# Kernel optimization log

Measured on AMD Instinct MI355X. Metric: run time of the kernel, lower is better.

## Reference

```python
import jax, jax.numpy as jnp
import numpy as np

BN_EPS = 1e-5
EPS = 1e-6


def _conv(x, w, pad, dil):
    # NCHW dilated conv, stride 1, no bias (matches nn.Conv2d(bias=False))
    return jax.lax.conv_general_dilated(
        x, w, window_strides=(1, 1), padding=[(pad, pad), (pad, pad)],
        rhs_dilation=(dil, dil), dimension_numbers=('NCHW', 'OIHW', 'NCHW'))


def _bn_relu(x, s, b, m, v):
    # eval-mode batchnorm (running stats) + relu
    inv = (s / jnp.sqrt(v + BN_EPS))[None, :, None, None]
    return jax.nn.relu((x - m[None, :, None, None]) * inv + b[None, :, None, None])


def _l2n(x):
    # l2_norm over channel dim (dim=-2 of [B,C,N]); no eps, as in source
    return x / jnp.linalg.norm(x, axis=1, keepdims=True)


def _forward(x, w1, w2, w3, w4, bn_scale, bn_bias, bn_mean, bn_var,
             wq, bq, wk, bk, wv, bv, gamma):
    B, C, H, W = x.shape
    N = H * W
    # HASP: four dilated-conv branches (dilations 1,6,12,18), concat to 128 ch
    specs = [(w1, 0, 1), (w2, 6, 6), (w3, 12, 12), (w4, 18, 18)]
    branches = [_bn_relu(_conv(x, w, p, d), bn_scale[i], bn_bias[i],
                         bn_mean[i], bn_var[i])
                for i, (w, p, d) in enumerate(specs)]
    x_q = jnp.concatenate(branches, axis=1)  # [B,128,H,W]
    # 1x1 convs as channel GEMMs
    Q = (jnp.einsum('oi,bihw->bohw', wq[:, :, 0, 0], x_q)
         + bq[None, :, None, None]).reshape(B, -1, N)  # [B,16,N]
    K = (jnp.einsum('oi,bihw->bohw', wk[:, :, 0, 0], x)
         + bk[None, :, None, None]).reshape(B, -1, N)  # [B,16,N]
    V = (jnp.einsum('oi,bihw->bohw', wv[:, :, 0, 0], x)
         + bv[None, :, None, None]).reshape(B, -1, N)  # [B,128,N]
    Qn = _l2n(Q).transpose(0, 2, 1)  # [B,N,16]
    Kn = _l2n(K)                     # [B,16,N]
    tailor = 1.0 / (N + jnp.einsum('bnm,bm->bn', Qn, Kn.sum(-1) + EPS))  # [B,N]
    vsum = V.sum(-1)[:, :, None]                      # [B,128,1]
    mat = jnp.einsum('bmn,bcn->bmc', Kn, V)           # [B,16,128]
    msum = vsum + jnp.einsum('bnm,bmc->bcn', Qn, mat)  # [B,128,N]
    out = (msum * tailor[:, None, :]).reshape(B, C, H, W)
    return gamma * out


def setup_inputs() -> dict:
    key = jax.random.key(0)
    ks = jax.random.split(key, 12)
    B, C, H, W = 8, 128, 128, 128
    M = 16  # in_places // scale
    d = {
        'x': jax.random.normal(ks[0], (B, C, H, W), jnp.float32),
        'w1': jax.random.normal(ks[1], (32, 128, 1, 1), jnp.float32) * 0.05,
        'w2': jax.random.normal(ks[2], (32, 128, 3, 3), jnp.float32) * 0.05,
        'w3': jax.random.normal(ks[3], (32, 128, 3, 3), jnp.float32) * 0.05,
        'w4': jax.random.normal(ks[4], (32, 128, 3, 3), jnp.float32) * 0.05,
        'bn_scale': jnp.ones((4, 32), jnp.float32),
        'bn_bias': jnp.zeros((4, 32), jnp.float32),
        'bn_mean': jnp.zeros((4, 32), jnp.float32),
        'bn_var': jnp.ones((4, 32), jnp.float32),
        'wq': jax.random.normal(ks[5], (M, 128, 1, 1), jnp.float32) * 0.05,
        'bq': jax.random.normal(ks[6], (M,), jnp.float32) * 0.05,
        'wk': jax.random.normal(ks[7], (M, 128, 1, 1), jnp.float32) * 0.05,
        'bk': jax.random.normal(ks[8], (M,), jnp.float32) * 0.05,
        'wv': jax.random.normal(ks[9], (C, 128, 1, 1), jnp.float32) * 0.05,
        'bv': jax.random.normal(ks[10], (C,), jnp.float32) * 0.05,
        'gamma': jax.random.uniform(ks[11], (1,), jnp.float32),
    }
    return d


def reference(x, w1, w2, w3, w4, bn_scale, bn_bias, bn_mean, bn_var,
              wq, bq, wk, bk, wv, bv, gamma):
    return _forward(x, w1, w2, w3, w4, bn_scale, bn_bias, bn_mean, bn_var,
                    wq, bq, wk, bk, wv, bv, gamma)
```

## Files before the change

kernel.cpp:

```cpp
#include <hip/hip_runtime.h>
#include <hip/hip_bf16.h>
#include <math.h>

#define NPIX   16384
#define BATCH  8
#define BN_EPS 1e-5f
#define EPS_V  1e-6f

typedef __attribute__((ext_vector_type(8))) short bf16x8;
typedef __attribute__((ext_vector_type(4))) float f32x4;
typedef const __attribute__((address_space(1))) unsigned int* gas_ptr;
typedef __attribute__((address_space(3))) unsigned int* las_ptr;

#define OFF_K     ((size_t)0)
#define OFF_PART2 ((size_t)8192)
#define OFF_W1F   ((size_t)2097152)
#define OFF_WKT   ((size_t)2101248)
#define OFF_WVT   ((size_t)2103296)
#define OFF_BF    ((size_t)2119680)
#define OFF_PART  ((size_t)2119808)
#define OFF_STATS ((size_t)3242112)
#define BASE_END  ((size_t)3259648)
#define OFF_WBT   BASE_END
#define OFF_XT    ((size_t)3314976)
#define OFF_WVB   ((size_t)11703584)
#define OFF_ZROW  ((size_t)11711776)
#define NEW_END   ((size_t)11713824)
#define OFF_W24T  BASE_END

__device__ inline unsigned short f2bf(float f) {
  union { float f; unsigned int u; } v; v.f = f;
  unsigned int r = (v.u + 0x7FFFu + ((v.u >> 16) & 1u)) >> 16;
  return (unsigned short)r;
}

__global__ void prep_common_kernel(const float* __restrict__ w1,
                                   const float* __restrict__ bns, const float* __restrict__ bnb,
                                   const float* __restrict__ bnm, const float* __restrict__ bnv,
                                   const float* __restrict__ wk, const float* __restrict__ wv,
                                   float* __restrict__ w1f, float* __restrict__ wkt,
                                   float* __restrict__ wvt, float* __restrict__ bf) {
  int tid = blockIdx.x * blockDim.x + threadIdx.x;
  int nt  = gridDim.x * blockDim.x;
  for (int i = tid; i < 128; i += nt) {
    float inv = bns[i] * rsqrtf(bnv[i] + BN_EPS);
    bf[i] = bnb[i] - bnm[i] * inv;
  }
  for (int i = tid; i < 4096; i += nt) {
    int c = i >> 5, o = i & 31;
    float inv = bns[o] * rsqrtf(bnv[o] + BN_EPS);
    w1f[i] = w1[o * 128 + c] * inv;
  }
  for (int i = tid; i < 2048; i += nt) {
    int c = i >> 4, m = i & 15;
    wkt[i] = wk[m * 128 + c];
  }
  for (int i = tid; i < 16384; i += nt) {
    int c = i >> 7, o = i & 127;
    wvt[i] = wv[o * 128 + c];
  }
}

__global__ void prep_convb_kernel(const float* __restrict__ w1,
                                  const float* __restrict__ w2, const float* __restrict__ w3,
                                  const float* __restrict__ w4,
                                  const float* __restrict__ bns, const float* __restrict__ bnv,
                                  const float* __restrict__ wk, const float* __restrict__ wv,
                                  unsigned short* __restrict__ wbtr,
                                  unsigned short* __restrict__ wvbr,
                                  unsigned short* __restrict__ wxbr,
                                  unsigned short* __restrict__ zrow) {
  int tid = blockIdx.x * blockDim.x + threadIdx.x;
  int nt  = gridDim.x * blockDim.x;
  for (int i = tid; i < 4096; i += nt) zrow[i] = 0;
  for (int i = tid; i < 16384; i += nt) {
    int e = i & 7, lane = (i >> 3) & 63, f = (i >> 9) & 7, q = i >> 12;
    int oc = f * 16 + (lane & 15);
    int c  = q * 32 + (lane >> 4) * 8 + e;
    wvbr[i] = f2bf(wv[oc * 128 + c]);
  }
  for (int i = tid; i < 6144; i += nt) {
    int e = i & 7, lane = (i >> 3) & 63, ct = i >> 9;
    int tile = ct % 3, q = ct / 3;
    int c = q * 32 + (lane >> 4) * 8 + e;
    float val;
    if (tile < 2) {
      int oc = tile * 16 + (lane & 15);
      val = w1[oc * 128 + c] * (bns[oc] * rsqrtf(bnv[oc] + BN_EPS));
    } else {
      val = wk[(lane & 15) * 128 + c];
    }
    wxbr[i] = f2bf(val);
  }
  for (int i = tid; i < 110592; i += nt) {
    int br = i / 36864;
    int r  = i - br * 36864;
    int tap  = r >> 12;
    int r2   = r & 4095;
    int q    = r2 >> 10;
    int r3   = r2 & 1023;
    int pair = r3 >> 9;
    int r4   = r3 & 511;
    int lane = r4 >> 3, e = r4 & 7;
    int oc = pair * 16 + (lane & 15);
    int c  = q * 32 + (lane >> 4) * 8 + e;
    const float* w = (br == 0) ? w2 : ((br == 1) ? w3 : w4);
    int bo = (br + 1) * 32 + oc;
    float inv = bns[bo] * rsqrtf(bnv[bo] + BN_EPS);
    wbtr[i] = f2bf(w[(oc * 128 + c) * 9 + tap] * inv);
  }
}

__global__ void prep_convf_kernel(const float* __restrict__ w2, const float* __restrict__ w3,
                                  const float* __restrict__ w4,
                                  const float* __restrict__ bns, const float* __restrict__ bnv,
                                  float* __restrict__ w24t) {
  int tid = blockIdx.x * blockDim.x + threadIdx.x;
  int nt  = gridDim.x * blockDim.x;
  for (int i = tid; i < 110592; i += nt) {
    int br  = i / 36864;
    int rem = i - br * 36864;
    int c   = rem / 288;
    int k   = (rem % 288) >> 5;
    int o   = rem & 31;
    const float* w = (br == 0) ? w2 : ((br == 1) ? w3 : w4);
    int bo = (br + 1) * 32 + o;
    float inv = bns[bo] * rsqrtf(bnv[bo] + BN_EPS);
    w24t[i] = w[(o * 128 + c) * 9 + k] * inv;
  }
}

__global__ __launch_bounds__(256) void a0_kernel(const float* __restrict__ x,
                                                 unsigned short* __restrict__ xt) {
  __shared__ unsigned short Ts[64][132];
  int t   = threadIdx.x;
  int b   = blockIdx.y;
  int px0 = blockIdx.x * 64;
  const float* xb = x + (size_t)b * 128 * NPIX;
  int p = t & 63, cq = t >> 6;
#pragma unroll 8
  for (int i = 0; i < 32; ++i) {
    int c = cq * 32 + i;
    Ts[p][c] = f2bf(xb[(size_t)c * NPIX + px0 + p]);
  }
  __syncthreads();
  int pw = t >> 2, cg = t & 3;
  unsigned short* dst = xt + ((size_t)(b * 4 + cg) * 16384 + px0 + pw) * 32;
  int sw = (pw >> 1) & 3;
#pragma unroll
  for (int k = 0; k < 8; ++k) {
    uint2 v = *(const uint2*)(&Ts[pw][cg * 32 + k * 4]);
    int cgs = (k >> 1) ^ sw;
    *(uint2*)(dst + cgs * 8 + (k & 1) * 4) = v;
  }
}

__global__ __launch_bounds__(256) void a1_kernel(const float* __restrict__ x,
                                                 const float* __restrict__ w1f,
                                                 const float* __restrict__ wkt,
                                                 const float* __restrict__ bfp,
                                                 const float* __restrict__ bk,
                                                 float* __restrict__ out,
                                                 float* __restrict__ Kbuf) {
  __shared__ float lw1[128 * 32];
  __shared__ float lwk[128 * 16];
  __shared__ float lbf[32];
  int t = threadIdx.x;
  for (int i = t; i < 4096; i += 256) lw1[i] = w1f[i];
  for (int i = t; i < 2048; i += 256) lwk[i] = wkt[i];
  if (t < 32) lbf[t] = bfp[t];
  __syncthreads();

  int b  = blockIdx.y;
  int px = blockIdx.x * 256 + t;
  const float* xb = x + (size_t)b * 128 * NPIX;

  float acc[48];
#pragma unroll
  for (int i = 0; i < 48; ++i) acc[i] = 0.f;

  for (int c = 0; c < 128; ++c) {
    float xv = xb[(size_t)c * NPIX + px];
    const float4* w1p = (const float4*)(lw1 + c * 32);
#pragma unroll
    for (int j = 0; j < 8; ++j) {
      float4 w = w1p[j];
      acc[j*4+0] = fmaf(w.x, xv, acc[j*4+0]);
      acc[j*4+1] = fmaf(w.y, xv, acc[j*4+1]);
      acc[j*4+2] = fmaf(w.z, xv, acc[j*4+2]);
      acc[j*4+3] = fmaf(w.w, xv, acc[j*4+3]);
    }
    const float4* wkp = (const float4*)(lwk + c * 16);
#pragma unroll
    for (int j = 0; j < 4; ++j) {
      float4 w = wkp[j];
      acc[32+j*4+0] = fmaf(w.x, xv, acc[32+j*4+0]);
      acc[32+j*4+1] = fmaf(w.y, xv, acc[32+j*4+1]);
      acc[32+j*4+2] = fmaf(w.z, xv, acc[32+j*4+2]);
      acc[32+j*4+3] = fmaf(w.w, xv, acc[32+j*4+3]);
    }
  }
#pragma unroll
  for (int o = 0; o < 32; ++o)
    out[((size_t)(b * 128 + o)) * NPIX + px] = fmaxf(acc[o] + lbf[o], 0.f);
#pragma unroll
  for (int m = 0; m < 16; ++m)
    Kbuf[((size_t)(b * 16 + m)) * NPIX + px] = acc[32 + m] + bk[m];
}

__global__ __launch_bounds__(256) void a2m_kernel(const unsigned short* __restrict__ xt,
                                                  const unsigned short* __restrict__ zrow,
                                                  const unsigned short* __restrict__ wbtr,
                                                  const float* __restrict__ bfp,
                                                  float* __restrict__ out) {
  __shared__ unsigned short sx[3 * 8192 + 8];
  int t    = threadIdx.x;
  int wave = t >> 6, lane = t & 63;
  int l15  = lane & 15, cg = lane >> 4;
  int idx  = blockIdx.x;
  int b    = idx & 7;
  int rest = idx >> 3;
  int h2   = rest & 63;
  int br   = rest >> 6;
  int d    = 6 * (br + 1);
  int h0   = h2 * 2;
  int j    = wave >> 1;
  int whalf = wave & 1;
  int p0   = whalf * 64;

  if (t == 0) *(uint4*)(sx + 24576) = make_uint4(0u, 0u, 0u, 0u);

  const unsigned short* wb    = wbtr + (size_t)br * 36864;
  const unsigned short* slabs = xt + (size_t)b * 4 * 524288;

  f32x4 acc[2][4];
#pragma unroll
  for (int i = 0; i < 2; ++i)
#pragma unroll
    for (int n = 0; n < 4; ++n) acc[i][n] = (f32x4){0.f, 0.f, 0.f, 0.f};

  int pxb[3], xorv[3];
#pragma unroll
  for (int kw = 0; kw < 3; ++kw) {
    pxb[kw]  = p0 + l15 + (kw - 1) * d;
    xorv[kw] = (cg ^ ((pxb[kw] >> 1) & 3)) << 4;
  }

  auto STAGE = [&](int s) {
    int q = s / 3, kh = s % 3;
    int srow = h0 + j + (kh - 1) * d;
    const unsigned short* rowsrc =
        ((unsigned)srow < 128u) ? (slabs + (size_t)q * 524288 + (size_t)srow * 4096)
                                : zrow;
    const unsigned short* gsrc = rowsrc + whalf * 2048 + lane * 8;
    unsigned short* lbase = sx + (s % 3) * 8192 + j * 4096 + whalf * 2048;
#pragma unroll
    for (int k = 0; k < 4; ++k)
      __builtin_amdgcn_global_load_lds((gas_ptr)(const void*)(gsrc + k * 512),
                                       (las_ptr)(void*)(lbase + k * 512), 16, 0, 0);
  };

  auto COMPUTE = [&](int s) {
    int q = s / 3, kh = s % 3;
    int bb = (s % 3) * 16384 + j * 8192;
    bf16x8 a[3][2];
#pragma unroll
    for (int kw = 0; kw < 3; ++kw) {
      int tap = kh * 3 + kw;
      const unsigned short* wt = wb + ((((size_t)tap * 4 + q) * 2) << 9);
      a[kw][0] = *(const bf16x8*)(wt + lane * 8);
      a[kw][1] = *(const bf16x8*)(wt + 512 + lane * 8);
    }
#pragma unroll
    for (int kw = 0; kw < 3; ++kw) {
      int base = bb + pxb[kw] * 64 + xorv[kw];
#pragma unroll
      for (int nf = 0; nf < 4; ++nf) {
        int px   = pxb[kw] + nf * 16;
        int addr = ((unsigned)px < 128u) ? (base + nf * 1024) : 49152;
        bf16x8 bv = *(const bf16x8*)((const char*)sx + addr);
        acc[0][nf] = __builtin_amdgcn_mfma_f32_16x16x32_bf16(a[kw][0], bv, acc[0][nf], 0, 0, 0);
        acc[1][nf] = __builtin_amdgcn_mfma_f32_16x16x32_bf16(a[kw][1], bv, acc[1][nf], 0, 0, 0);
      }
    }
  };

  STAGE(0);
  STAGE(1);
  __syncthreads();
  for (int s = 0; s < 12; ++s) {
    COMPUTE(s);
    if (s < 10) STAGE(s + 2);
    if (s < 11) {
      if (s < 10) asm volatile("s_waitcnt vmcnt(4)" ::: "memory");
      else        asm volatile("s_waitcnt vmcnt(0)" ::: "memory");
      __builtin_amdgcn_s_barrier();
      __builtin_amdgcn_sched_barrier(0);
    }
  }

  int ocb = (br + 1) * 32;
  int pxw = (h0 + j) * 128 + p0;
#pragma unroll
  for (int mf = 0; mf < 2; ++mf) {
#pragma unroll
    for (int r = 0; r < 4; ++r) {
      int oc = mf * 16 + cg * 4 + r;
      float bias = bfp[ocb + oc];
      float* op = out + ((size_t)(b * 128 + ocb + oc)) * NPIX + pxw + l15;
#pragma unroll
      for (int nf = 0; nf < 4; ++nf)
        op[nf * 16] = fmaxf(acc[mf][nf][r] + bias, 0.f);
    }
  }
}

__global__ __launch_bounds__(256) void a2f_kernel(const float* __restrict__ x,
                                                  const float* __restrict__ w24t,
                                                  const float* __restrict__ bfp,
                                                  float* __restrict__ out) {
  int t  = threadIdx.x;
  int og = t & 3;
  int pg = (t >> 2) & 15;
  int r  = t >> 6;
  int br = blockIdx.z;
  int b  = blockIdx.y;
  int h  = blockIdx.x * 4 + r;
  int d  = 6 * (br + 1);

  const float* wt = w24t + (size_t)br * 36864;
  const float* bf = bfp + (br + 1) * 32;
  const float* xb = x + (size_t)b * 128 * NPIX;
  int w0 = pg << 3;

  float acc[8][8];
#pragma unroll
  for (int p = 0; p < 8; ++p)
#pragma unroll
    for (int o = 0; o < 8; ++o) acc[p][o] = 0.f;

  for (int c = 0; c < 128; ++c) {
    const float* xc = xb + (size_t)c * NPIX;
    const float* wc = wt + c * 288;
#pragma unroll
    for (int kh = 0; kh < 3; ++kh) {
      int row = h + (kh - 1) * d;
      if ((unsigned)row >= 128u) continue;
      const float* xr = xc + row * 128;
#pragma unroll
      for (int kw = 0; kw < 3; ++kw) {
        int wb = w0 + (kw - 1) * d;
        float xv[8];
        if (wb >= 0 && wb <= 120) {
          const float2* p2 = (const float2*)(xr + wb);
#pragma unroll
          for (int jj = 0; jj < 4; ++jj) {
            float2 v = p2[jj];
            xv[2*jj] = v.x; xv[2*jj+1] = v.y;
          }
        } else {
#pragma unroll
          for (int jj = 0; jj < 8; ++jj) {
            int ww = wb + jj;
            xv[jj] = ((unsigned)ww < 128u) ? xr[ww] : 0.f;
          }
        }
        const float4* wp = (const float4*)(wc + (kh * 3 + kw) * 32 + og * 8);
        float4 wa = wp[0], wbv = wp[1];
        float wr[8] = {wa.x, wa.y, wa.z, wa.w, wbv.x, wbv.y, wbv.z, wbv.w};
#pragma unroll
        for (int p = 0; p < 8; ++p)
#pragma unroll
          for (int o = 0; o < 8; ++o)
            acc[p][o] = fmaf(xv[p], wr[o], acc[p][o]);
      }
    }
  }

  int chbase = (br + 1) * 32 + og * 8;
  int n = h * 128 + w0;
#pragma unroll
  for (int o = 0; o < 8; ++o) {
    float bias = bf[og * 8 + o];
    float* op = out + ((size_t)(b * 128 + chbase + o)) * NPIX + n;
    float4 v0 = make_float4(fmaxf(acc[0][o] + bias, 0.f), fmaxf(acc[1][o] + bias, 0.f),
                            fmaxf(acc[2][o] + bias, 0.f), fmaxf(acc[3][o] + bias, 0.f));
    float4 v1 = make_float4(fmaxf(acc[4][o] + bias, 0.f), fmaxf(acc[5][o] + bias, 0.f),
                            fmaxf(acc[6][o] + bias, 0.f), fmaxf(acc[7][o] + bias, 0.f));
    ((float4*)op)[0] = v0;
    ((float4*)op)[1] = v1;
  }
}

__global__ __launch_bounds__(256) void cm_kernel(const unsigned short* __restrict__ xt,
                                                 const unsigned short* __restrict__ wvbr,
                                                 const unsigned short* __restrict__ wxbr,
                                                 const float* __restrict__ bv,
                                                 const float* __restrict__ bfp,
                                                 const float* __restrict__ bk,
                                                 float* __restrict__ out,
                                                 float* __restrict__ part1,
                                                 float* __restrict__ part2) {
  __shared__ __align__(16) unsigned short Vl[128 * 136];
  __shared__ __align__(16) unsigned short knl[16 * 136];
  int t    = threadIdx.x;
  int idx  = blockIdx.x;
  int b    = idx & 7;
  int blk  = idx >> 3;
  int wave = t >> 6, lane = t & 63;
  int l15  = lane & 15, cg = lane >> 4;
  int ocb  = wave * 32;
  int pbase = blk << 7;
  int cgsw = (cg ^ ((l15 >> 1) & 3)) << 3;

  float bvr[2][4];
#pragma unroll
  for (int mf = 0; mf < 2; ++mf)
#pragma unroll
    for (int r = 0; r < 4; ++r) bvr[mf][r] = bv[ocb + mf * 16 + cg * 4 + r];

  float xb4[4];
#pragma unroll
  for (int r = 0; r < 4; ++r) xb4[r] = 0.f;
  if (wave == 0) {
#pragma unroll
    for (int r = 0; r < 4; ++r) xb4[r] = bfp[cg * 4 + r];
  } else if (wave == 1) {
#pragma unroll
    for (int r = 0; r < 4; ++r) xb4[r] = bfp[16 + cg * 4 + r];
  } else if (wave == 2) {
#pragma unroll
    for (int r = 0; r < 4; ++r) xb4[r] = bk[cg * 4 + r];
  }
  int xwave = (wave < 3) ? wave : 0;

  float kr[4] = {0.f, 0.f, 0.f, 0.f};
  float sv[2][4];
#pragma unroll
  for (int mf = 0; mf < 2; ++mf)
#pragma unroll
    for (int r = 0; r < 4; ++r) sv[mf][r] = 0.f;
  f32x4 am[2];
  am[0] = (f32x4){0.f,0.f,0.f,0.f};
  am[1] = (f32x4){0.f,0.f,0.f,0.f};

#pragma unroll
  for (int hf = 0; hf < 2; ++hf) {
    f32x4 vacc[2][4];
    f32x4 xacc[4];
#pragma unroll
    for (int i = 0; i < 2; ++i)
#pragma unroll
      for (int n = 0; n < 4; ++n) vacc[i][n] = (f32x4){0.f,0.f,0.f,0.f};
#pragma unroll
    for (int n = 0; n < 4; ++n) xacc[n] = (f32x4){0.f,0.f,0.f,0.f};

#pragma unroll
    for (int cc = 0; cc < 4; ++cc) {
      const unsigned short* xq = xt + ((size_t)(b * 4 + cc) * 16384 + pbase) * 32;
      bf16x8 a0 = *(const bf16x8*)(wvbr + ((cc * 8 + wave * 2 + 0) << 9) + lane * 8);
      bf16x8 a1 = *(const bf16x8*)(wvbr + ((cc * 8 + wave * 2 + 1) << 9) + lane * 8);
      bf16x8 ax = *(const bf16x8*)(wxbr + ((cc * 3 + xwave) << 9) + lane * 8);
#pragma unroll
      for (int nf = 0; nf < 4; ++nf) {
        int nfg = hf * 4 + nf;
        bf16x8 bx = *(const bf16x8*)(xq + (size_t)(nfg * 16 + l15) * 32 + cgsw);
        vacc[0][nf] = __builtin_amdgcn_mfma_f32_16x16x32_bf16(a0, bx, vacc[0][nf], 0, 0, 0);
        vacc[1][nf] = __builtin_amdgcn_mfma_f32_16x16x32_bf16(a1, bx, vacc[1][nf], 0, 0, 0);
        if (wave < 3)
          xacc[nf] = __builtin_amdgcn_mfma_f32_16x16x32_bf16(ax, bx, xacc[nf], 0, 0, 0);
      }
    }

#pragma unroll
    for (int mf = 0; mf < 2; ++mf) {
#pragma unroll
      for (int r = 0; r < 4; ++r) {
        float s = 0.f;
#pragma unroll
        for (int nf = 0; nf < 4; ++nf) s += vacc[mf][nf][r];
        sv[mf][r] += s;
        int c = ocb + mf * 16 + cg * 4 + r;
#pragma unroll
        for (int nf = 0; nf < 4; ++nf)
          Vl[c * 136 + (hf * 4 + nf) * 16 + l15] = f2bf(vacc[mf][nf][r] + bvr[mf][r]);
      }
    }

    if (wave < 2) {
#pragma unroll
      for (int r = 0; r < 4; ++r) {
        int oc = wave * 16 + cg * 4 + r;
        float* op = out + ((size_t)(b * 128 + oc)) * NPIX + pbase + l15;
#pragma unroll
        for (int nf = 0; nf < 4; ++nf)
          op[(hf * 4 + nf) * 16] = fmaxf(xacc[nf][r] + xb4[r], 0.f);
      }
    } else if (wave == 2) {
#pragma unroll
      for (int nf = 0; nf < 4; ++nf) {
        int nfg = hf * 4 + nf;
        float kq[4]; float s2 = 0.f;
#pragma unroll
        for (int r = 0; r < 4; ++r) {
          kq[r] = xacc[nf][r] + xb4[r];
          s2 = fmaf(kq[r], kq[r], s2);
        }
        s2 += __shfl_xor(s2, 16);
        s2 += __shfl_xor(s2, 32);
        float inv = rsqrtf(s2);
#pragma unroll
        for (int r = 0; r < 4; ++r) {
          float kn = kq[r] * inv;
          knl[(cg * 4 + r) * 136 + nfg * 16 + l15] = f2bf(kn);
          kr[r] += kn;
        }
      }
    }
  }
  __syncthreads();

#pragma unroll
  for (int ks = 0; ks < 4; ++ks) {
    bf16x8 af = *(const bf16x8*)(knl + l15 * 136 + ks * 32 + cg * 8);
    bf16x8 b0 = *(const bf16x8*)(Vl + (size_t)(ocb + l15) * 136 + ks * 32 + cg * 8);
    bf16x8 b1 = *(const bf16x8*)(Vl + (size_t)(ocb + 16 + l15) * 136 + ks * 32 + cg * 8);
    am[0] = __builtin_amdgcn_mfma_f32_16x16x32_bf16(af, b0, am[0], 0, 0, 0);
    am[1] = __builtin_amdgcn_mfma_f32_16x16x32_bf16(af, b1, am[1], 0, 0, 0);
  }

  float* pp = (blk < 64) ? (part1 + ((size_t)b * 64 + blk) * 2192)
                         : (part2 + ((size_t)b * 64 + (blk - 64)) * 2192);
#pragma unroll
  for (int nf2 = 0; nf2 < 2; ++nf2)
#pragma unroll
    for (int r = 0; r < 4; ++r)
      pp[(cg * 4 + r) * 128 + ocb + nf2 * 16 + l15] = am[nf2][r];
#pragma unroll
  for (int off = 1; off < 16; off <<= 1) {
#pragma unroll
    for (int mf = 0; mf < 2; ++mf)
#pragma unroll
      for (int r = 0; r < 4; ++r)
        sv[mf][r] += __shfl_xor(sv[mf][r], off);
  }
  if (l15 == 0) {
#pragma unroll
    for (int mf = 0; mf < 2; ++mf)
#pragma unroll
      for (int r = 0; r < 4; ++r) {
        int c = ocb + mf * 16 + cg * 4 + r;
        pp[2048 + c] = sv[mf][r] + 128.f * bv[c];
      }
  }
  if (wave == 2) {
#pragma unroll
    for (int off = 1; off < 16; off <<= 1) {
#pragma unroll
      for (int r = 0; r < 4; ++r)
        kr[r] += __shfl_xor(kr[r], off);
    }
    if (l15 == 0) {
#pragma unroll
      for (int r = 0; r < 4; ++r)
        pp[2048 + 128 + cg * 4 + r] = kr[r];
    }
  }
}

__global__ __launch_bounds__(256) void cf_kernel(const float* __restrict__ x,
                                                 const float* __restrict__ bv,
                                                 const float* __restrict__ Kbuf,
                                                 const float* __restrict__ wvt,
                                                 float* __restrict__ part) {
  __shared__ float Vl[128 * 129];
  __shared__ float knl[16 * 132];
  int t   = threadIdx.x;
  int b   = blockIdx.y;
  int blk = blockIdx.x;
  const float* Kb = Kbuf + (size_t)b * 16 * NPIX;
  const float* xb = x + (size_t)b * 128 * NPIX;

  int m_own = t & 15;
  int c0    = (t >> 4) << 3;
  int pxg   = t & 15;

  float bvr[8];
#pragma unroll
  for (int jj = 0; jj < 8; ++jj) bvr[jj] = bv[c0 + jj];

  float macc[8] = {0,0,0,0,0,0,0,0};
  float vs[8]   = {0,0,0,0,0,0,0,0};
  float ksum[16];
#pragma unroll
  for (int m = 0; m < 16; ++m) ksum[m] = 0.f;

  for (int tile = blk; tile < 128; tile += 64) {
    __syncthreads();
    int pbase = tile << 7;

    if (t < 128) {
      float kv[16]; float ss = 0.f;
#pragma unroll
      for (int m = 0; m < 16; ++m) {
        kv[m] = Kb[(size_t)m * NPIX + pbase + t];
        ss = fmaf(kv[m], kv[m], ss);
      }
      float inv = rsqrtf(ss);
#pragma unroll
      for (int m = 0; m < 16; ++m) {
        float kn = kv[m] * inv;
        knl[m * 132 + t] = kn;
        ksum[m] += kn;
      }
    }

    float v[8][8];
#pragma unroll
    for (int i = 0; i < 8; ++i)
// ... 125 lines not shown
#pragma unroll
  for (int m = 0; m < 16; ++m) q[m] *= inv;
  float den = (float)NPIX;
#pragma unroll
  for (int m = 0; m < 16; ++m) den = fmaf(q[m], ksl[m], den);
  float tl = gamma[0] / den;

  for (int c = 0; c < 128; ++c) {
    float s = vsl[c];
    const float4* mp = (const float4*)(matl + c * 16);
#pragma unroll
    for (int jj = 0; jj < 4; ++jj) {
      float4 w = mp[jj];
      s = fmaf(w.x, q[jj*4+0], s);
      s = fmaf(w.y, q[jj*4+1], s);
      s = fmaf(w.z, q[jj*4+2], s);
      s = fmaf(w.w, q[jj*4+3], s);
    }
    ob[(size_t)c * NPIX + px] = tl * s;
  }
}

extern "C" void kernel_launch(void* const* d_in, const int* in_sizes, int n_in,
                              void* d_out, int out_size, void* d_ws, size_t ws_size,
                              hipStream_t stream) {
  (void)in_sizes; (void)n_in; (void)out_size;
  const float* x   = (const float*)d_in[0];
  const float* w1  = (const float*)d_in[1];
  const float* w2  = (const float*)d_in[2];
  const float* w3  = (const float*)d_in[3];
  const float* w4  = (const float*)d_in[4];
  const float* bns = (const float*)d_in[5];
  const float* bnb = (const float*)d_in[6];
  const float* bnm = (const float*)d_in[7];
  const float* bnv = (const float*)d_in[8];
  const float* wq  = (const float*)d_in[9];
  const float* bq  = (const float*)d_in[10];
  const float* wk  = (const float*)d_in[11];
  const float* bk  = (const float*)d_in[12];
  const float* wv  = (const float*)d_in[13];
  const float* bv  = (const float*)d_in[14];
  const float* gm  = (const float*)d_in[15];
  float* ws  = (float*)d_ws;
  float* out = (float*)d_out;

  float* Kbuf = ws + OFF_K;
  float* w1f  = ws + OFF_W1F;
  float* wkt  = ws + OFF_WKT;
  float* wvt  = ws + OFF_WVT;
  float* bfp  = ws + OFF_BF;
  float* part = ws + OFF_PART;
  float* stat = ws + OFF_STATS;

  prep_common_kernel<<<64, 256, 0, stream>>>(w1, bns, bnb, bnm, bnv, wk, wv,
                                             w1f, wkt, wvt, bfp);

  bool use_mfma = ws_size >= NEW_END * sizeof(float);
  if (use_mfma) {
    unsigned short* wbtr = (unsigned short*)(ws + OFF_WBT);
    unsigned short* xt   = (unsigned short*)(ws + OFF_XT);
    unsigned short* wvbr = (unsigned short*)(ws + OFF_WVB);
    unsigned short* zrow = (unsigned short*)(ws + OFF_ZROW);
    unsigned short* wxbr = (unsigned short*)(ws + OFF_K);
    float* part2 = ws + OFF_PART2;
    prep_convb_kernel<<<64, 256, 0, stream>>>(w1, w2, w3, w4, bns, bnv, wk, wv,
                                              wbtr, wvbr, wxbr, zrow);
    a0_kernel<<<dim3(256, 8), 256, 0, stream>>>(x, xt);
    a2m_kernel<<<dim3(1536), 256, 0, stream>>>(xt, zrow, wbtr, bfp, out);
    cm_kernel<<<dim3(1024), 256, 0, stream>>>(xt, wvbr, wxbr, bv, bfp, bk, out, part, part2);
    reduce2_kernel<<<dim3(9, 8), 256, 0, stream>>>(part, part2, stat);
    df_kernel<<<dim3(64, 8), 256, 0, stream>>>(stat, wq, bq, gm, out);
  } else {
    float* w24t = ws + OFF_W24T;
    prep_convf_kernel<<<64, 256, 0, stream>>>(w2, w3, w4, bns, bnv, w24t);
    a1_kernel<<<dim3(64, 8), 256, 0, stream>>>(x, w1f, wkt, bfp, bk, out, Kbuf);
    a2f_kernel<<<dim3(32, 8, 3), 256, 0, stream>>>(x, w24t, bfp, out);
    cf_kernel<<<dim3(64, 8), 256, 0, stream>>>(x, bv, Kbuf, wvt, part);
    reduce_kernel<<<dim3(9, 8), 256, 0, stream>>>(part, stat);
    df_kernel<<<dim3(64, 8), 256, 0, stream>>>(stat, wq, bq, gm, out);
  }
}
```

Baseline: 138.5 us.

## Merge prep with transpose and dilated-conv with channel GEMM kernels to cut launches

Result: slower. 142.6 us (+3.0%).

```diff
diff --git a/kernel.cpp b/kernel.cpp
--- a/kernel.cpp
+++ b/kernel.cpp
@@ -61,53 +61,90 @@
   }
 }
 
-__global__ void prep_convb_kernel(const float* __restrict__ w1,
-                                  const float* __restrict__ w2, const float* __restrict__ w3,
-                                  const float* __restrict__ w4,
-                                  const float* __restrict__ bns, const float* __restrict__ bnv,
-                                  const float* __restrict__ wk, const float* __restrict__ wv,
-                                  unsigned short* __restrict__ wbtr,
-                                  unsigned short* __restrict__ wvbr,
-                                  unsigned short* __restrict__ wxbr,
-                                  unsigned short* __restrict__ zrow) {
-  int tid = blockIdx.x * blockDim.x + threadIdx.x;
-  int nt  = gridDim.x * blockDim.x;
-  for (int i = tid; i < 4096; i += nt) zrow[i] = 0;
-  for (int i = tid; i < 16384; i += nt) {
-    int e = i & 7, lane = (i >> 3) & 63, f = (i >> 9) & 7, q = i >> 12;
-    int oc = f * 16 + (lane & 15);
-    int c  = q * 32 + (lane >> 4) * 8 + e;
-    wvbr[i] = f2bf(wv[oc * 128 + c]);
-  }
-  for (int i = tid; i < 6144; i += nt) {
-    int e = i & 7, lane = (i >> 3) & 63, ct = i >> 9;
-    int tile = ct % 3, q = ct / 3;
-    int c = q * 32 + (lane >> 4) * 8 + e;
-    float val;
-    if (tile < 2) {
-      int oc = tile * 16 + (lane & 15);
-      val = w1[oc * 128 + c] * (bns[oc] * rsqrtf(bnv[oc] + BN_EPS));
-    } else {
-      val = wk[(lane & 15) * 128 + c];
-    }
-    wxbr[i] = f2bf(val);
-  }
-  for (int i = tid; i < 110592; i += nt) {
-    int br = i / 36864;
-    int r  = i - br * 36864;
-    int tap  = r >> 12;
-    int r2   = r & 4095;
-    int q    = r2 >> 10;
-    int r3   = r2 & 1023;
-    int pair = r3 >> 9;
-    int r4   = r3 & 511;
-    int lane = r4 >> 3, e = r4 & 7;
-    int oc = pair * 16 + (lane & 15);
-    int c  = q * 32 + (lane >> 4) * 8 + e;
-    const float* w = (br == 0) ? w2 : ((br == 1) ? w3 : w4);
-    int bo = (br + 1) * 32 + oc;
-    float inv = bns[bo] * rsqrtf(bnv[bo] + BN_EPS);
-    wbtr[i] = f2bf(w[(oc * 128 + c) * 9 + tap] * inv);
+__global__ __launch_bounds__(256) void pa0_kernel(const float* __restrict__ x,
+                                                  unsigned short* __restrict__ xt,
+                                                  const float* __restrict__ w1,
+                                                  const float* __restrict__ w2,
+                                                  const float* __restrict__ w3,
+                                                  const float* __restrict__ w4,
+                                                  const float* __restrict__ bns,
+                                                  const float* __restrict__ bnb,
+                                                  const float* __restrict__ bnm,
+                                                  const float* __restrict__ bnv,
+                                                  const float* __restrict__ wk,
+                                                  const float* __restrict__ wv,
+                                                  unsigned short* __restrict__ wbtr,
+                                                  unsigned short* __restrict__ wvbr,
+                                                  unsigned short* __restrict__ wxbr,
+                                                  unsigned short* __restrict__ zrow,
+                                                  float* __restrict__ bf) {
+  __shared__ unsigned short Ts[64][132];
+  int t   = threadIdx.x;
+  int idx = blockIdx.x;
+  if (idx < 2048) {
+    int b   = idx & 7;
+    int px0 = (idx >> 3) * 64;
+    const float* xb = x + (size_t)b * 128 * NPIX;
+    int p = t & 63, cq = t >> 6;
+#pragma unroll 8
+    for (int i = 0; i < 32; ++i) {
+      int c = cq * 32 + i;
+      Ts[p][c] = f2bf(xb[(size_t)c * NPIX + px0 + p]);
+    }
+    __syncthreads();
+    int pw = t >> 2, cg = t & 3;
+    unsigned short* dst = xt + ((size_t)(b * 4 + cg) * 16384 + px0 + pw) * 32;
+    int sw = (pw >> 1) & 3;
+#pragma unroll
+    for (int k = 0; k < 8; ++k) {
+      uint2 v = *(const uint2*)(&Ts[pw][cg * 32 + k * 4]);
+      int cgs = (k >> 1) ^ sw;
+      *(uint2*)(dst + cgs * 8 + (k & 1) * 4) = v;
+    }
+  } else {
+    int tid = (idx - 2048) * 256 + t;
+    int nt  = 64 * 256;
+    for (int i = tid; i < 128; i += nt) {
+      float inv = bns[i] * rsqrtf(bnv[i] + BN_EPS);
+      bf[i] = bnb[i] - bnm[i] * inv;
+    }
+    for (int i = tid; i < 4096; i += nt) zrow[i] = 0;
+    for (int i = tid; i < 16384; i += nt) {
+      int e = i & 7, lane = (i >> 3) & 63, f = (i >> 9) & 7, q = i >> 12;
+      int oc = f * 16 + (lane & 15);
+      int c  = q * 32 + (lane >> 4) * 8 + e;
+      wvbr[i] = f2bf(wv[oc * 128 + c]);
+    }
+    for (int i = tid; i < 6144; i += nt) {
+      int e = i & 7, lane = (i >> 3) & 63, ct = i >> 9;
+      int tile = ct % 3, q = ct / 3;
+      int c = q * 32 + (lane >> 4) * 8 + e;
+      float val;
+      if (tile < 2) {
+        int oc = tile * 16 + (lane & 15);
+        val = w1[oc * 128 + c] * (bns[oc] * rsqrtf(bnv[oc] + BN_EPS));
+      } else {
+        val = wk[(lane & 15) * 128 + c];
+      }
+      wxbr[i] = f2bf(val);
+    }
+    for (int i = tid; i < 110592; i += nt) {
+      int br = i / 36864;
+      int r  = i - br * 36864;
+      int tap  = r >> 12;
+      int r2   = r & 4095;
+      int q    = r2 >> 10;
+      int r3   = r2 & 1023;
+      int pair = r3 >> 9;
+      int r4   = r3 & 511;
+      int lane = r4 >> 3, e = r4 & 7;
+      int oc = pair * 16 + (lane & 15);
+      int c  = q * 32 + (lane >> 4) * 8 + e;
+      const float* w = (br == 0) ? w2 : ((br == 1) ? w3 : w4);
+      int bo = (br + 1) * 32 + oc;
+      float inv = bns[bo] * rsqrtf(bnv[bo] + BN_EPS);
+      wbtr[i] = f2bf(w[(oc * 128 + c) * 9 + tap] * inv);
+    }
   }
 }
 
@@ -130,31 +167,6 @@
   }
 }
 
-__global__ __launch_bounds__(256) void a0_kernel(const float* __restrict__ x,
-                                                 unsigned short* __restrict__ xt) {
-  __shared__ unsigned short Ts[64][132];
-  int t   = threadIdx.x;
-  int b   = blockIdx.y;
-  int px0 = blockIdx.x * 64;
-  const float* xb = x + (size_t)b * 128 * NPIX;
-  int p = t & 63, cq = t >> 6;
-#pragma unroll 8
-  for (int i = 0; i < 32; ++i) {
-    int c = cq * 32 + i;
-    Ts[p][c] = f2bf(xb[(size_t)c * NPIX + px0 + p]);
-  }
-  __syncthreads();
-  int pw = t >> 2, cg = t & 3;
-  unsigned short* dst = xt + ((size_t)(b * 4 + cg) * 16384 + px0 + pw) * 32;
-  int sw = (pw >> 1) & 3;
-#pragma unroll
-  for (int k = 0; k < 8; ++k) {
-    uint2 v = *(const uint2*)(&Ts[pw][cg * 32 + k * 4]);
-    int cgs = (k >> 1) ^ sw;
-    *(uint2*)(dst + cgs * 8 + (k & 1) * 4) = v;
-  }
-}
-
 __global__ __launch_bounds__(256) void a1_kernel(const float* __restrict__ x,
                                                  const float* __restrict__ w1f,
                                                  const float* __restrict__ wkt,
@@ -208,109 +220,282 @@
     Kbuf[((size_t)(b * 16 + m)) * NPIX + px] = acc[32 + m] + bk[m];
 }
 
-__global__ __launch_bounds__(256) void a2m_kernel(const unsigned short* __restrict__ xt,
-                                                  const unsigned short* __restrict__ zrow,
-                                                  const unsigned short* __restrict__ wbtr,
-                                                  const float* __restrict__ bfp,
-                                                  float* __restrict__ out) {
-  __shared__ unsigned short sx[3 * 8192 + 8];
-  int t    = threadIdx.x;
+__global__ __launch_bounds__(256) void ac_kernel(const unsigned short* __restrict__ xt,
+                                                 const unsigned short* __restrict__ zrow,
+                                                 const unsigned short* __restrict__ wbtr,
+                                                 const unsigned short* __restrict__ wvbr,
+                                                 const unsigned short* __restrict__ wxbr,
+                                                 const float* __restrict__ bv,
+                                                 const float* __restrict__ bfp,
+                                                 const float* __restrict__ bk,
+                                                 float* __restrict__ out,
+                                                 float* __restrict__ part1,
+                                                 float* __restrict__ part2) {
+  __shared__ __align__(16) char smem[49168];
+  int t = threadIdx.x;
   int wave = t >> 6, lane = t & 63;
   int l15  = lane & 15, cg = lane >> 4;
-  int idx  = blockIdx.x;
-  int b    = idx & 7;
-  int rest = idx >> 3;
-  int h2   = rest & 63;
-  int br   = rest >> 6;
-  int d    = 6 * (br + 1);
-  int h0   = h2 * 2;
-  int j    = wave >> 1;
-  int whalf = wave & 1;
-  int p0   = whalf * 64;
-
-  if (t == 0) *(uint4*)(sx + 24576) = make_uint4(0u, 0u, 0u, 0u);
-
-  const unsigned short* wb    = wbtr + (size_t)br * 36864;
-  const unsigned short* slabs = xt + (size_t)b * 4 * 524288;
-
-  f32x4 acc[2][4];
-#pragma unroll
-  for (int i = 0; i < 2; ++i)
-#pragma unroll
-    for (int n = 0; n < 4; ++n) acc[i][n] = (f32x4){0.f, 0.f, 0.f, 0.f};
-
-  int pxb[3], xorv[3];
-#pragma unroll
-  for (int kw = 0; kw < 3; ++kw) {
-    pxb[kw]  = p0 + l15 + (kw - 1) * d;
-    xorv[kw] = (cg ^ ((pxb[kw] >> 1) & 3)) << 4;
-  }
-
-  auto STAGE = [&](int s) {
-    int q = s / 3, kh = s % 3;
-    int srow = h0 + j + (kh - 1) * d;
-    const unsigned short* rowsrc =
-        ((unsigned)srow < 128u) ? (slabs + (size_t)q * 524288 + (size_t)srow * 4096)
-                                : zrow;
-    const unsigned short* gsrc = rowsrc + whalf * 2048 + lane * 8;
-    unsigned short* lbase = sx + (s % 3) * 8192 + j * 4096 + whalf * 2048;
-#pragma unroll
-    for (int k = 0; k < 4; ++k)
-      __builtin_amdgcn_global_load_lds((gas_ptr)(const void*)(gsrc + k * 512),
-                                       (las_ptr)(void*)(lbase + k * 512), 16, 0, 0);
-  };
-
-  auto COMPUTE = [&](int s) {
-    int q = s / 3, kh = s % 3;
-    int bb = (s % 3) * 16384 + j * 8192;
-    bf16x8 a[3][2];
+
+  if (blockIdx.x < 1536) {
+    unsigned short* sx = (unsigned short*)smem;
+    int idx  = blockIdx.x;
+    int b    = idx & 7;
+    int rest = idx >> 3;
+    int h2   = rest & 63;
+    int br   = rest >> 6;
+    int d    = 6 * (br + 1);
+    int h0   = h2 * 2;
+    int j    = wave >> 1;
+    int whalf = wave & 1;
+    int p0   = whalf * 64;
+
+    if (t == 0) *(uint4*)(sx + 24576) = make_uint4(0u, 0u, 0u, 0u);
+
+    const unsigned short* wb    = wbtr + (size_t)br * 36864;
+    const unsigned short* slabs = xt + (size_t)b * 4 * 524288;
+
+    f32x4 acc[2][4];
+#pragma unroll
+    for (int i = 0; i < 2; ++i)
+#pragma unroll
+      for (int n = 0; n < 4; ++n) acc[i][n] = (f32x4){0.f, 0.f, 0.f, 0.f};
+
+    int pxb[3], xorv[3];
 #pragma unroll
     for (int kw = 0; kw < 3; ++kw) {
-      int tap = kh * 3 + kw;
-      const unsigned short* wt = wb + ((((size_t)tap * 4 + q) * 2) << 9);
-      a[kw][0] = *(const bf16x8*)(wt + lane * 8);
-      a[kw][1] = *(const bf16x8*)(wt + 512 + lane * 8);
-    }
-#pragma unroll
-    for (int kw = 0; kw < 3; ++kw) {
-      int base = bb + pxb[kw] * 64 + xorv[kw];
-#pragma unroll
-      for (int nf = 0; nf < 4; ++nf) {
-        int px   = pxb[kw] + nf * 16;
-        int addr = ((unsigned)px < 128u) ? (base + nf * 1024) : 49152;
-        bf16x8 bv = *(const bf16x8*)((const char*)sx + addr);
-        acc[0][nf] = __builtin_amdgcn_mfma_f32_16x16x32_bf16(a[kw][0], bv, acc[0][nf], 0, 0, 0);
-        acc[1][nf] = __builtin_amdgcn_mfma_f32_16x16x32_bf16(a[kw][1], bv, acc[1][nf], 0, 0, 0);
-      }
-    }
-  };
-
-  STAGE(0);
-  STAGE(1);
-  __syncthreads();
-  for (int s = 0; s < 12; ++s) {
-    COMPUTE(s);
-    if (s < 10) STAGE(s + 2);
-    if (s < 11) {
-      if (s < 10) asm volatile("s_waitcnt vmcnt(4)" ::: "memory");
-      else        asm volatile("s_waitcnt vmcnt(0)" ::: "memory");
-      __builtin_amdgcn_s_barrier();
-      __builtin_amdgcn_sched_barrier(0);
-    }
-  }
-
-  int ocb = (br + 1) * 32;
-  int pxw = (h0 + j) * 128 + p0;
-#pragma unroll
-  for (int mf = 0; mf < 2; ++mf) {
-#pragma unroll
-    for (int r = 0; r < 4; ++r) {
-      int oc = mf * 16 + cg * 4 + r;
-      float bias = bfp[ocb + oc];
-      float* op = out + ((size_t)(b * 128 + ocb + oc)) * NPIX + pxw + l15;
-#pragma unroll
-      for (int nf = 0; nf < 4; ++nf)
-        op[nf * 16] = fmaxf(acc[mf][nf][r] + bias, 0.f);
+      pxb[kw]  = p0 + l15 + (kw - 1) * d;
+      xorv[kw] = (cg ^ ((pxb[kw] >> 1) & 3)) << 4;
+    }
+
+    auto STAGE = [&](int s) {
+      int q = s / 3, kh = s % 3;
+      int srow = h0 + j + (kh - 1) * d;
+      const unsigned short* rowsrc =
+          ((unsigned)srow < 128u) ? (slabs + (size_t)q * 524288 + (size_t)srow * 4096)
+                                  : zrow;
+      const unsigned short* gsrc = rowsrc + whalf * 2048 + lane * 8;
+      unsigned short* lbase = sx + (s % 3) * 8192 + j * 4096 + whalf * 2048;
+#pragma unroll
+      for (int k = 0; k < 4; ++k)
+        __builtin_amdgcn_global_load_lds((gas_ptr)(const void*)(gsrc + k * 512),
+                                         (las_ptr)(void*)(lbase + k * 512), 16, 0, 0);
+    };
+
+    auto COMPUTE = [&](int s) {
+      int q = s / 3, kh = s % 3;
+      int bb = (s % 3) * 16384 + j * 8192;
+      bf16x8 a[3][2];
+#pragma unroll
+      for (int kw = 0; kw < 3; ++kw) {
+        int tap = kh * 3 + kw;
+        const unsigned short* wt = wb + ((((size_t)tap * 4 + q) * 2) << 9);
+        a[kw][0] = *(const bf16x8*)(wt + lane * 8);
+        a[kw][1] = *(const bf16x8*)(wt + 512 + lane * 8);
+      }
+#pragma unroll
+      for (int kw = 0; kw < 3; ++kw) {
+        int base = bb + pxb[kw] * 64 + xorv[kw];
+#pragma unroll
+        for (int nf = 0; nf < 4; ++nf) {
+          int px   = pxb[kw] + nf * 16;
+          int addr = ((unsigned)px < 128u) ? (base + nf * 1024) : 49152;
+          bf16x8 bvv = *(const bf16x8*)((const char*)sx + addr);
+          acc[0][nf] = __builtin_amdgcn_mfma_f32_16x16x32_bf16(a[kw][0], bvv, acc[0][nf], 0, 0, 0);
+          acc[1][nf] = __builtin_amdgcn_mfma_f32_16x16x32_bf16(a[kw][1], bvv, acc[1][nf], 0, 0, 0);
+        }
+      }
+    };
+
+    STAGE(0);
+    STAGE(1);
+    __syncthreads();
+    for (int s = 0; s < 12; ++s) {
+      COMPUTE(s);
+      if (s < 10) STAGE(s + 2);
+      if (s < 11) {
+        if (s < 10) asm volatile("s_waitcnt vmcnt(4)" ::: "memory");
+        else        asm volatile("s_waitcnt vmcnt(0)" ::: "memory");
+        __builtin_amdgcn_s_barrier();
+        __builtin_amdgcn_sched_barrier(0);
+      }
+    }
+
+    int ocb = (br + 1) * 32;
+    int pxw = (h0 + j) * 128 + p0;
+#pragma unroll
+    for (int mf = 0; mf < 2; ++mf) {
+#pragma unroll
+      for (int r = 0; r < 4; ++r) {
+        int oc = mf * 16 + cg * 4 + r;
+        float bias = bfp[ocb + oc];
+        float* op = out + ((size_t)(b * 128 + ocb + oc)) * NPIX + pxw + l15;
+#pragma unroll
+        for (int nf = 0; nf < 4; ++nf)
+          op[nf * 16] = fmaxf(acc[mf][nf][r] + bias, 0.f);
+      }
+    }
+  } else {
+    unsigned short* Vl  = (unsigned short*)smem;
+    unsigned short* knl = (unsigned short*)(smem + 34816);
+    int idx2 = blockIdx.x - 1536;
+    int b    = idx2 & 7;
+    int blk  = idx2 >> 3;
+    int ocb  = wave * 32;
+    int pbase = blk << 7;
+    int cgsw = (cg ^ ((l15 >> 1) & 3)) << 3;
+
+    float bvr[2][4];
+#pragma unroll
+    for (int mf = 0; mf < 2; ++mf)
+#pragma unroll
+      for (int r = 0; r < 4; ++r) bvr[mf][r] = bv[ocb + mf * 16 + cg * 4 + r];
+
+    float xb4[4];
+#pragma unroll
+    for (int r = 0; r < 4; ++r) xb4[r] = 0.f;
+    if (wave == 0) {
+#pragma unroll
+      for (int r = 0; r < 4; ++r) xb4[r] = bfp[cg * 4 + r];
+    } else if (wave == 1) {
+#pragma unroll
+      for (int r = 0; r < 4; ++r) xb4[r] = bfp[16 + cg * 4 + r];
+    } else if (wave == 2) {
+#pragma unroll
+      for (int r = 0; r < 4; ++r) xb4[r] = bk[cg * 4 + r];
+    }
+    int xwave = (wave < 3) ? wave : 0;
+
+    float kr[4] = {0.f, 0.f, 0.f, 0.f};
+    float sv[2][4];
+#pragma unroll
+    for (int mf = 0; mf < 2; ++mf)
+#pragma unroll
+      for (int r = 0; r < 4; ++r) sv[mf][r] = 0.f;
+    f32x4 am[2];
+    am[0] = (f32x4){0.f,0.f,0.f,0.f};
+    am[1] = (f32x4){0.f,0.f,0.f,0.f};
+
+#pragma unroll
+    for (int hf = 0; hf < 2; ++hf) {
+      f32x4 vacc[2][4];
+      f32x4 xacc[4];
+#pragma unroll
+      for (int i = 0; i < 2; ++i)
+#pragma unroll
+        for (int n = 0; n < 4; ++n) vacc[i][n] = (f32x4){0.f,0.f,0.f,0.f};
+#pragma unroll
+      for (int n = 0; n < 4; ++n) xacc[n] = (f32x4){0.f,0.f,0.f,0.f};
+
+#pragma unroll
+      for (int cc = 0; cc < 4; ++cc) {
+        const unsigned short* xq = xt + ((size_t)(b * 4 + cc) * 16384 + pbase) * 32;
+        bf16x8 a0 = *(const bf16x8*)(wvbr + ((cc * 8 + wave * 2 + 0) << 9) + lane * 8);
+        bf16x8 a1 = *(const bf16x8*)(wvbr + ((cc * 8 + wave * 2 + 1) << 9) + lane * 8);
+        bf16x8 ax = *(const bf16x8*)(wxbr + ((cc * 3 + xwave) << 9) + lane * 8);
+#pragma unroll
+        for (int nf = 0; nf < 4; ++nf) {
+          int nfg = hf * 4 + nf;
+          bf16x8 bx = *(const bf16x8*)(xq + (size_t)(nfg * 16 + l15) * 32 + cgsw);
+          vacc[0][nf] = __builtin_amdgcn_mfma_f32_16x16x32_bf16(a0, bx, vacc[0][nf], 0, 0, 0);
+          vacc[1][nf] = __builtin_amdgcn_mfma_f32_16x16x32_bf16(a1, bx, vacc[1][nf], 0, 0, 0);
+          if (wave < 3)
+            xacc[nf] = __builtin_amdgcn_mfma_f32_16x16x32_bf16(ax, bx, xacc[nf], 0, 0, 0);
+        }
+      }
+
+#pragma unroll
+      for (int mf = 0; mf < 2; ++mf) {
+#pragma unroll
+        for (int r = 0; r < 4; ++r) {
+          float s = 0.f;
+#pragma unroll
+          for (int nf = 0; nf < 4; ++nf) s += vacc[mf][nf][r];
+          sv[mf][r] += s;
+          int c = ocb + mf * 16 + cg * 4 + r;
+#pragma unroll
+          for (int nf = 0; nf < 4; ++nf)
+            Vl[c * 136 + (hf * 4 + nf) * 16 + l15] = f2bf(vacc[mf][nf][r] + bvr[mf][r]);
+        }
+      }
+
+      if (wave < 2) {
+#pragma unroll
+        for (int r = 0; r < 4; ++r) {
+          int oc = wave * 16 + cg * 4 + r;
+          float* op = out + ((size_t)(b * 128 + oc)) * NPIX + pbase + l15;
+#pragma unroll
+          for (int nf = 0; nf < 4; ++nf)
+            op[(hf * 4 + nf) * 16] = fmaxf(xacc[nf][r] + xb4[r], 0.f);
+        }
+      } else if (wave == 2) {
+#pragma unroll
+        for (int nf = 0; nf < 4; ++nf) {
+          int nfg = hf * 4 + nf;
+          float kq[4]; float s2 = 0.f;
+#pragma unroll
+          for (int r = 0; r < 4; ++r) {
+            kq[r] = xacc[nf][r] + xb4[r];
+            s2 = fmaf(kq[r], kq[r], s2);
+          }
+          s2 += __shfl_xor(s2, 16);
+          s2 += __shfl_xor(s2, 32);
+          float inv = rsqrtf(s2);
+#pragma unroll
+          for (int r = 0; r < 4; ++r) {
+            float kn = kq[r] * inv;
+            knl[(cg * 4 + r) * 136 + nfg * 16 + l15] = f2bf(kn);
+            kr[r] += kn;
+          }
+        }
+      }
+    }
+    __syncthreads();
+
+#pragma unroll
+    for (int ks = 0; ks < 4; ++ks) {
+      bf16x8 af = *(const bf16x8*)(knl + l15 * 136 + ks * 32 + cg * 8);
+      bf16x8 b0 = *(const bf16x8*)(Vl + (size_t)(ocb + l15) * 136 + ks * 32 + cg * 8);
+      bf16x8 b1 = *(const bf16x8*)(Vl + (size_t)(ocb + 16 + l15) * 136 + ks * 32 + cg * 8);
+      am[0] = __builtin_amdgcn_mfma_f32_16x16x32_bf16(af, b0, am[0], 0, 0, 0);
+      am[1] = __builtin_amdgcn_mfma_f32_16x16x32_bf16(af, b1, am[1], 0, 0, 0);
+    }
+
+    float* pp = (blk < 64) ? (part1 + ((size_t)b * 64 + blk) * 2192)
+                           : (part2 + ((size_t)b * 64 + (blk - 64)) * 2192);
+#pragma unroll
+    for (int nf2 = 0; nf2 < 2; ++nf2)
+#pragma unroll
+      for (int r = 0; r < 4; ++r)
+        pp[(cg * 4 + r) * 128 + ocb + nf2 * 16 + l15] = am[nf2][r];
+#pragma unroll
+    for (int off = 1; off < 16; off <<= 1) {
+#pragma unroll
+      for (int mf = 0; mf < 2; ++mf)
+#pragma unroll
+        for (int r = 0; r < 4; ++r)
+          sv[mf][r] += __shfl_xor(sv[mf][r], off);
+    }
+    if (l15 == 0) {
+#pragma unroll
+      for (int mf = 0; mf < 2; ++mf)
+#pragma unroll
+        for (int r = 0; r < 4; ++r) {
+          int c = ocb + mf * 16 + cg * 4 + r;
+          pp[2048 + c] = sv[mf][r] + 128.f * bv[c];
+        }
+    }
+    if (wave == 2) {
+#pragma unroll
+      for (int off = 1; off < 16; off <<= 1) {
+#pragma unroll
+        for (int r = 0; r < 4; ++r)
+          kr[r] += __shfl_xor(kr[r], off);
+      }
+      if (l15 == 0) {
+#pragma unroll
+        for (int r = 0; r < 4; ++r)
+          pp[2048 + 128 + cg * 4 + r] = kr[r];
+      }
     }
   }
 }
@@ -389,182 +574,6 @@
                             fmaxf(acc[6][o] + bias, 0.f), fmaxf(acc[7][o] + bias, 0.f));
     ((float4*)op)[0] = v0;
     ((float4*)op)[1] = v1;
-  }
-}
-
-__global__ __launch_bounds__(256) void cm_kernel(const unsigned short* __restrict__ xt,
-                                                 const unsigned short* __restrict__ wvbr,
-                                                 const unsigned short* __restrict__ wxbr,
-                                                 const float* __restrict__ bv,
-                                                 const float* __restrict__ bfp,
-                                                 const float* __restrict__ bk,
-                                                 float* __restrict__ out,
-                                                 float* __restrict__ part1,
-                                                 float* __restrict__ part2) {
-  __shared__ __align__(16) unsigned short Vl[128 * 136];
-  __shared__ __align__(16) unsigned short knl[16 * 136];
-  int t    = threadIdx.x;
-  int idx  = blockIdx.x;
-  int b    = idx & 7;
-  int blk  = idx >> 3;
-  int wave = t >> 6, lane = t & 63;
-  int l15  = lane & 15, cg = lane >> 4;
-  int ocb  = wave * 32;
-  int pbase = blk << 7;
-  int cgsw = (cg ^ ((l15 >> 1) & 3)) << 3;
-
-  float bvr[2][4];
-#pragma unroll
-  for (int mf = 0; mf < 2; ++mf)
-#pragma unroll
-    for (int r = 0; r < 4; ++r) bvr[mf][r] = bv[ocb + mf * 16 + cg * 4 + r];
-
-  float xb4[4];
-#pragma unroll
-  for (int r = 0; r < 4; ++r) xb4[r] = 0.f;
-  if (wave == 0) {
-#pragma unroll
-    for (int r = 0; r < 4; ++r) xb4[r] = bfp[cg * 4 + r];
-  } else if (wave == 1) {
-#pragma unroll
-    for (int r = 0; r < 4; ++r) xb4[r] = bfp[16 + cg * 4 + r];
-  } else if (wave == 2) {
-#pragma unroll
-    for (int r = 0; r < 4; ++r) xb4[r] = bk[cg * 4 + r];
-  }
-  int xwave = (wave < 3) ? wave : 0;
-
-  float kr[4] = {0.f, 0.f, 0.f, 0.f};
-  float sv[2][4];
-#pragma unroll
-  for (int mf = 0; mf < 2; ++mf)
-#pragma unroll
-    for (int r = 0; r < 4; ++r) sv[mf][r] = 0.f;
-  f32x4 am[2];
-  am[0] = (f32x4){0.f,0.f,0.f,0.f};
-  am[1] = (f32x4){0.f,0.f,0.f,0.f};
-
-#pragma unroll
-  for (int hf = 0; hf < 2; ++hf) {
-    f32x4 vacc[2][4];
-    f32x4 xacc[4];
-#pragma unroll
-    for (int i = 0; i < 2; ++i)
-#pragma unroll
-      for (int n = 0; n < 4; ++n) vacc[i][n] = (f32x4){0.f,0.f,0.f,0.f};
-#pragma unroll
-    for (int n = 0; n < 4; ++n) xacc[n] = (f32x4){0.f,0.f,0.f,0.f};
-
-#pragma unroll
-    for (int cc = 0; cc < 4; ++cc) {
-      const unsigned short* xq = xt + ((size_t)(b * 4 + cc) * 16384 + pbase) * 32;
-      bf16x8 a0 = *(const bf16x8*)(wvbr + ((cc * 8 + wave * 2 + 0) << 9) + lane * 8);
-      bf16x8 a1 = *(const bf16x8*)(wvbr + ((cc * 8 + wave * 2 + 1) << 9) + lane * 8);
-      bf16x8 ax = *(const bf16x8*)(wxbr + ((cc * 3 + xwave) << 9) + lane * 8);
-#pragma unroll
-      for (int nf = 0; nf < 4; ++nf) {
-        int nfg = hf * 4 + nf;
-        bf16x8 bx = *(const bf16x8*)(xq + (size_t)(nfg * 16 + l15) * 32 + cgsw);
-        vacc[0][nf] = __builtin_amdgcn_mfma_f32_16x16x32_bf16(a0, bx, vacc[0][nf], 0, 0, 0);
-        vacc[1][nf] = __builtin_amdgcn_mfma_f32_16x16x32_bf16(a1, bx, vacc[1][nf], 0, 0, 0);
-        if (wave < 3)
-          xacc[nf] = __builtin_amdgcn_mfma_f32_16x16x32_bf16(ax, bx, xacc[nf], 0, 0, 0);
-      }
-    }
-
-#pragma unroll
-    for (int mf = 0; mf < 2; ++mf) {
-#pragma unroll
-      for (int r = 0; r < 4; ++r) {
-        float s = 0.f;
-#pragma unroll
-        for (int nf = 0; nf < 4; ++nf) s += vacc[mf][nf][r];
-        sv[mf][r] += s;
-        int c = ocb + mf * 16 + cg * 4 + r;
-#pragma unroll
-        for (int nf = 0; nf < 4; ++nf)
-          Vl[c * 136 + (hf * 4 + nf) * 16 + l15] = f2bf(vacc[mf][nf][r] + bvr[mf][r]);
-      }
-    }
-
-    if (wave < 2) {
-#pragma unroll
-      for (int r = 0; r < 4; ++r) {
-        int oc = wave * 16 + cg * 4 + r;
-        float* op = out + ((size_t)(b * 128 + oc)) * NPIX + pbase + l15;
-#pragma unroll
-        for (int nf = 0; nf < 4; ++nf)
-          op[(hf * 4 + nf) * 16] = fmaxf(xacc[nf][r] + xb4[r], 0.f);
-      }
-    } else if (wave == 2) {
-#pragma unroll
-      for (int nf = 0; nf < 4; ++nf) {
-        int nfg = hf * 4 + nf;
-        float kq[4]; float s2 = 0.f;
-#pragma unroll
-        for (int r = 0; r < 4; ++r) {
-          kq[r] = xacc[nf][r] + xb4[r];
-          s2 = fmaf(kq[r], kq[r], s2);
-        }
-        s2 += __shfl_xor(s2, 16);
-        s2 += __shfl_xor(s2, 32);
-        float inv = rsqrtf(s2);
-#pragma unroll
-        for (int r = 0; r < 4; ++r) {
-          float kn = kq[r] * inv;
-          knl[(cg * 4 + r) * 136 + nfg * 16 + l15] = f2bf(kn);
-          kr[r] += kn;
-        }
-      }
-    }
-  }
-  __syncthreads();
-
-#pragma unroll
-  for (int ks = 0; ks < 4; ++ks) {
-    bf16x8 af = *(const bf16x8*)(knl + l15 * 136 + ks * 32 + cg * 8);
-    bf16x8 b0 = *(const bf16x8*)(Vl + (size_t)(ocb + l15) * 136 + ks * 32 + cg * 8);
-    bf16x8 b1 = *(const bf16x8*)(Vl + (size_t)(ocb + 16 + l15) * 136 + ks * 32 + cg * 8);
-    am[0] = __builtin_amdgcn_mfma_f32_16x16x32_bf16(af, b0, am[0], 0, 0, 0);
-    am[1] = __builtin_amdgcn_mfma_f32_16x16x32_bf16(af, b1, am[1], 0, 0, 0);
-  }
-
-  float* pp = (blk < 64) ? (part1 + ((size_t)b * 64 + blk) * 2192)
-                         : (part2 + ((size_t)b * 64 + (blk - 64)) * 2192);
-#pragma unroll
-  for (int nf2 = 0; nf2 < 2; ++nf2)
-#pragma unroll
-    for (int r = 0; r < 4; ++r)
-      pp[(cg * 4 + r) * 128 + ocb + nf2 * 16 + l15] = am[nf2][r];
-#pragma unroll
-  for (int off = 1; off < 16; off <<= 1) {
-#pragma unroll
-    for (int mf = 0; mf < 2; ++mf)
-#pragma unroll
-      for (int r = 0; r < 4; ++r)
-        sv[mf][r] += __shfl_xor(sv[mf][r], off);
-  }
-  if (l15 == 0) {
-#pragma unroll
-    for (int mf = 0; mf < 2; ++mf)
-#pragma unroll
-      for (int r = 0; r < 4; ++r) {
-        int c = ocb + mf * 16 + cg * 4 + r;
-        pp[2048 + c] = sv[mf][r] + 128.f * bv[c];
-      }
-  }
-  if (wave == 2) {
-#pragma unroll
-    for (int off = 1; off < 16; off <<= 1) {
-#pragma unroll
-      for (int r = 0; r < 4; ++r)
-        kr[r] += __shfl_xor(kr[r], off);
-    }
-    if (l15 == 0) {
-#pragma unroll
-      for (int r = 0; r < 4; ++r)
-        pp[2048 + 128 + cg * 4 + r] = kr[r];
-    }
   }
 }
 
@@ -796,9 +805,6 @@
   float* part = ws + OFF_PART;
   float* stat = ws + OFF_STATS;
 
-  prep_common_kernel<<<64, 256, 0, stream>>>(w1, bns, bnb, bnm, bnv, wk, wv,
-                                             w1f, wkt, wvt, bfp);
-
   bool use_mfma = ws_size >= NEW_END * sizeof(float);
   if (use_mfma) {
     unsigned short* wbtr = (unsigned short*)(ws + OFF_WBT);
@@ -807,15 +813,17 @@
     unsigned short* zrow = (unsigned short*)(ws + OFF_ZROW);
     unsigned short* wxbr = (unsigned short*)(ws + OFF_K);
     float* part2 = ws + OFF_PART2;
-    prep_convb_kernel<<<64, 256, 0, stream>>>(w1, w2, w3, w4, bns, bnv, wk, wv,
-                                              wbtr, wvbr, wxbr, zrow);
-    a0_kernel<<<dim3(256, 8), 256, 0, stream>>>(x, xt);
-    a2m_kernel<<<dim3(1536), 256, 0, stream>>>(xt, zrow, wbtr, bfp, out);
-    cm_kernel<<<dim3(1024), 256, 0, stream>>>(xt, wvbr, wxbr, bv, bfp, bk, out, part, part2);
+    pa0_kernel<<<dim3(2112), 256, 0, stream>>>(x, xt, w1, w2, w3, w4,
+                                               bns, bnb, bnm, bnv, wk, wv,
+                                               wbtr, wvbr, wxbr, zrow, bfp);
+    ac_kernel<<<dim3(2560), 256, 0, stream>>>(xt, zrow, wbtr, wvbr, wxbr,
+                                              bv, bfp, bk, out, part, part2);
     reduce2_kernel<<<dim3(9, 8), 256, 0, stream>>>(part, part2, stat);
     df_kernel<<<dim3(64, 8), 256, 0, stream>>>(stat, wq, bq, gm, out);
   } else {
     float* w24t = ws + OFF_W24T;
+    prep_common_kernel<<<64, 256, 0, stream>>>(w1, bns, bnb, bnm, bnv, wk, wv,
+                                               w1f, wkt, wvt, bfp);
     prep_convf_kernel<<<64, 256, 0, stream>>>(w2, w3, w4, bns, bnv, w24t);
     a1_kernel<<<dim3(64, 8), 256, 0, stream>>>(x, w1f, wkt, bfp, bk, out, Kbuf);
     a2f_kernel<<<dim3(32, 8, 3), 256, 0, stream>>>(x, w24t, bfp, out);
```
